# Performance work log

Hardware: AMD Instinct MI355X
Metric: run time of the kernel (lower is better)

Reference implementation:

```python
import jax, jax.numpy as jnp
import numpy as np

SIGMA_SPATIAL = 1.0
SIGMA_BILATERAL = 0.25
RADIUS = 1
PATCH = 2 * RADIUS + 1  # 3


def _spatial_kernel():
    x, y = np.mgrid[-RADIUS:RADIUS + 1, -RADIUS:RADIUS + 1]
    w1 = np.exp(-(x ** 2 + y ** 2) / (2.0 * SIGMA_SPATIAL ** 2))
    return jnp.asarray(w1.reshape(-1), dtype=jnp.float32)  # [PATCH*PATCH]


def _extract_patches(x):
    # x: [B,H,W,C] -> [B,H,W,PATCH*PATCH,C] via reflect-padded shifted slices
    B, H, W, C = x.shape
    xp = jnp.pad(x, ((0, 0), (RADIUS, RADIUS), (RADIUS, RADIUS), (0, 0)), mode='reflect')
    return jnp.stack(
        [xp[:, dy:dy + H, dx:dx + W, :] for dy in range(PATCH) for dx in range(PATCH)],
        axis=3,
    )


def setup_inputs() -> dict:
    key = jax.random.key(0)
    k1, k2 = jax.random.split(key)
    src = jax.random.uniform(k1, (2, 512, 512, 21), dtype=jnp.float32)
    im = jax.random.uniform(k2, (2, 512, 512, 3), dtype=jnp.float32)
    return {"src": src, "im": im}


def reference(src, im):
    w1 = _spatial_kernel()  # [9]
    im_patches = _extract_patches(im)                      # [B,H,W,9,Ci]
    diff2 = jnp.sum((im_patches - im[:, :, :, None, :]) ** 2, axis=-1)  # [B,H,W,9]
    w = jnp.exp(-diff2 / (2.0 * SIGMA_BILATERAL ** 2)) * w1            # [B,H,W,9]
    src_patches = _extract_patches(src)                    # [B,H,W,9,Cs]
    num = jnp.sum(src_patches * w[..., None], axis=3)      # [B,H,W,Cs]
    den = jnp.sum(w, axis=3, keepdims=True)                # [B,H,W,1]
    return num / den
```

## Files before the change

kernel.cpp:

```cpp
#include <hip/hip_runtime.h>

#define BATCH 2
#define H 512
#define W 512
#define CS 21
#define CI 3
#define P 64
#define TPB 256

__device__ __forceinline__ int reflect1(int v, int n) {
    if (v < 0) v = -v;
    else if (v >= n) v = 2 * n - 2 - v;
    return v;
}

__global__ __launch_bounds__(TPB) void jbu_kernel(
    const float* __restrict__ src, const float* __restrict__ im,
    float* __restrict__ out)
{
    __shared__ float s_im[3][P + 2][CI];
    __shared__ float s_w[P * 9];
    __shared__ float s_invden[P];

    const int t  = threadIdx.x;
    const int x0 = blockIdx.x * P;
    const int y  = blockIdx.y;
    const int b  = blockIdx.z;

    const int ry0 = reflect1(y - 1, H);
    const int ry2 = reflect1(y + 1, H);
    const int ryr[3] = { ry0, y, ry2 };

    for (int i = t; i < 3 * (P + 2) * CI; i += TPB) {
        int r   = i / ((P + 2) * CI);
        int rem = i - r * ((P + 2) * CI);
        int col = rem / CI;
        int ch  = rem - col * CI;
        int gx  = reflect1(x0 + col - 1, W);
        s_im[r][col][ch] = im[((b * H + ryr[r]) * W + gx) * CI + ch];
    }
    __syncthreads();

    const float w1[9] = {0.36787944f, 0.60653066f, 0.36787944f,
                         0.60653066f, 1.0f,        0.60653066f,
                         0.36787944f, 0.60653066f, 0.36787944f};

    for (int s = t; s < P * 9; s += TPB) {
        int p  = s / 9;
        int k  = s - p * 9;
        int dy = k / 3;
        int dx = k - dy * 3;
        float d0 = s_im[dy][p + dx][0] - s_im[1][p + 1][0];
        float d1 = s_im[dy][p + dx][1] - s_im[1][p + 1][1];
        float d2 = s_im[dy][p + dx][2] - s_im[1][p + 1][2];
        float dist2 = d0 * d0 + d1 * d1 + d2 * d2;
        s_w[s] = __expf(-8.0f * dist2) * w1[k];
    }
    __syncthreads();

    if (t < P) {
        float den = 0.f;
        #pragma unroll
        for (int k = 0; k < 9; ++k) den += s_w[t * 9 + k];
        s_invden[t] = 1.0f / den;
    }
    __syncthreads();

    const long rowb0 = (long)(b * H + ry0) * W;
    const long rowb1 = (long)(b * H + y  ) * W;
    const long rowb2 = (long)(b * H + ry2) * W;

    for (int e = t; e < P * CS; e += TPB) {
        int p = e / CS;
        int c = e - p * CS;
        int x = x0 + p;
        int xm = reflect1(x - 1, W);
        int xp = reflect1(x + 1, W);
        const float* wp = &s_w[p * 9];
        float acc;
        acc  = src[(rowb0 + xm) * CS + c] * wp[0];
        acc += src[(rowb0 + x ) * CS + c] * wp[1];
        acc += src[(rowb0 + xp) * CS + c] * wp[2];
        acc += src[(rowb1 + xm) * CS + c] * wp[3];
        acc += src[(rowb1 + x ) * CS + c] * wp[4];
        acc += src[(rowb1 + xp) * CS + c] * wp[5];
        acc += src[(rowb2 + xm) * CS + c] * wp[6];
        acc += src[(rowb2 + x ) * CS + c] * wp[7];
        acc += src[(rowb2 + xp) * CS + c] * wp[8];
        out[(rowb1 + x) * CS + c] = acc * s_invden[p];
    }
}

extern "C" void kernel_launch(void* const* d_in, const int* in_sizes, int n_in,
                              void* d_out, int out_size, void* d_ws, size_t ws_size,
                              hipStream_t stream) {
    const float* src = (const float*)d_in[0];
    const float* im  = (const float*)d_in[1];
    float* out = (float*)d_out;
    dim3 grid(W / P, H, BATCH);
    jbu_kernel<<<grid, TPB, 0, stream>>>(src, im, out);
}
```

Baseline: 126.1 us.

## Vectorize source stencil with float4 chunks and fold normalization into weights

Each block now covers 256 pixels instead of 64, so one thread owns one pixel. Each thread computes its 9 bilateral weights and their normalized values in registers, which removes a separate denominator pass and one barrier. The gather of the 21 source channels becomes 6 float4 chunks per pixel, with the last chunk starting at channel 17 and overlapping the previous one. The goal is to cut the number of global load and store instructions and the redundant scalar index arithmetic. Because 21 channels is odd, the float4 accesses are not 16-byte aligned, so this relies on the hardware handling unaligned vector loads and stores. Channels 17 to 19 are also written twice with identical values.

```diff
diff --git a/kernel.cpp b/kernel.cpp
--- a/kernel.cpp
+++ b/kernel.cpp
@@ -5,8 +5,9 @@
 #define W 512
 #define CS 21
 #define CI 3
-#define P 64
+#define P 256
 #define TPB 256
+#define NCH 6
 
 __device__ __forceinline__ int reflect1(int v, int n) {
     if (v < 0) v = -v;
@@ -14,13 +15,19 @@
     return v;
 }
 
+__device__ __forceinline__ void fma4(float4& a, const float4 v, const float w) {
+    a.x = fmaf(v.x, w, a.x);
+    a.y = fmaf(v.y, w, a.y);
+    a.z = fmaf(v.z, w, a.z);
+    a.w = fmaf(v.w, w, a.w);
+}
+
 __global__ __launch_bounds__(TPB) void jbu_kernel(
     const float* __restrict__ src, const float* __restrict__ im,
     float* __restrict__ out)
 {
-    __shared__ float s_im[3][P + 2][CI];
-    __shared__ float s_w[P * 9];
-    __shared__ float s_invden[P];
+    __shared__ __align__(16) float s_im[3][P + 2][CI];
+    __shared__ __align__(16) float s_w[P][12];
 
     const int t  = threadIdx.x;
     const int x0 = blockIdx.x * P;
@@ -29,65 +36,88 @@
 
     const int ry0 = reflect1(y - 1, H);
     const int ry2 = reflect1(y + 1, H);
-    const int ryr[3] = { ry0, y, ry2 };
 
     for (int i = t; i < 3 * (P + 2) * CI; i += TPB) {
         int r   = i / ((P + 2) * CI);
         int rem = i - r * ((P + 2) * CI);
         int col = rem / CI;
         int ch  = rem - col * CI;
+        int ry  = (r == 0) ? ry0 : ((r == 1) ? y : ry2);
         int gx  = reflect1(x0 + col - 1, W);
-        s_im[r][col][ch] = im[((b * H + ryr[r]) * W + gx) * CI + ch];
+        s_im[r][col][ch] = im[((b * H + ry) * W + gx) * CI + ch];
     }
     __syncthreads();
 
-    const float w1[9] = {0.36787944f, 0.60653066f, 0.36787944f,
-                         0.60653066f, 1.0f,        0.60653066f,
-                         0.36787944f, 0.60653066f, 0.36787944f};
-
-    for (int s = t; s < P * 9; s += TPB) {
-        int p  = s / 9;
-        int k  = s - p * 9;
-        int dy = k / 3;
-        int dx = k - dy * 3;
-        float d0 = s_im[dy][p + dx][0] - s_im[1][p + 1][0];
-        float d1 = s_im[dy][p + dx][1] - s_im[1][p + 1][1];
-        float d2 = s_im[dy][p + dx][2] - s_im[1][p + 1][2];
-        float dist2 = d0 * d0 + d1 * d1 + d2 * d2;
-        s_w[s] = __expf(-8.0f * dist2) * w1[k];
+    {
+        const float w1k[9] = {0.36787944f, 0.60653066f, 0.36787944f,
+                              0.60653066f, 1.0f,        0.60653066f,
+                              0.36787944f, 0.60653066f, 0.36787944f};
+        const float c0 = s_im[1][t + 1][0];
+        const float c1 = s_im[1][t + 1][1];
+        const float c2 = s_im[1][t + 1][2];
+        float wv[9];
+        float den = 0.f;
+        #pragma unroll
+        for (int k = 0; k < 9; ++k) {
+            const int dy = k / 3, dx = k % 3;
+            float d0 = s_im[dy][t + dx][0] - c0;
+            float d1 = s_im[dy][t + dx][1] - c1;
+            float d2 = s_im[dy][t + dx][2] - c2;
+            float w = __expf(-8.0f * (d0 * d0 + d1 * d1 + d2 * d2)) * w1k[k];
+            wv[k] = w;
+            den += w;
+        }
+        const float inv = 1.0f / den;
+        float4 wa = {wv[0] * inv, wv[1] * inv, wv[2] * inv, wv[3] * inv};
+        float4 wb = {wv[4] * inv, wv[5] * inv, wv[6] * inv, wv[7] * inv};
+        *(float4*)&s_w[t][0] = wa;
+        *(float4*)&s_w[t][4] = wb;
+        s_w[t][8] = wv[8] * inv;
     }
     __syncthreads();
 
-    if (t < P) {
-        float den = 0.f;
-        #pragma unroll
-        for (int k = 0; k < 9; ++k) den += s_w[t * 9 + k];
-        s_invden[t] = 1.0f / den;
-    }
-    __syncthreads();
+    const float* row0 = src + (size_t)(b * H + ry0) * (W * CS);
+    const float* row1 = src + (size_t)(b * H + y  ) * (W * CS);
+    const float* row2 = src + (size_t)(b * H + ry2) * (W * CS);
+    float*       orow = out + (size_t)(b * H + y  ) * (W * CS);
 
-    const long rowb0 = (long)(b * H + ry0) * W;
-    const long rowb1 = (long)(b * H + y  ) * W;
-    const long rowb2 = (long)(b * H + ry2) * W;
+    for (int wi = t; wi < P * NCH; wi += TPB) {
+        int p = wi / NCH;
+        int q = wi - p * NCH;
+        int coff = (q == 5) ? 17 : (q << 2);
+        int x  = x0 + p;
+        int xm = (x == 0)     ? 1     : x - 1;
+        int xp = (x == W - 1) ? W - 2 : x + 1;
+        int om = xm * CS + coff;
+        int oc = x  * CS + coff;
+        int op = xp * CS + coff;
 
-    for (int e = t; e < P * CS; e += TPB) {
-        int p = e / CS;
-        int c = e - p * CS;
-        int x = x0 + p;
-        int xm = reflect1(x - 1, W);
-        int xp = reflect1(x + 1, W);
-        const float* wp = &s_w[p * 9];
-        float acc;
-        acc  = src[(rowb0 + xm) * CS + c] * wp[0];
-        acc += src[(rowb0 + x ) * CS + c] * wp[1];
-        acc += src[(rowb0 + xp) * CS + c] * wp[2];
-        acc += src[(rowb1 + xm) * CS + c] * wp[3];
-        acc += src[(rowb1 + x ) * CS + c] * wp[4];
-        acc += src[(rowb1 + xp) * CS + c] * wp[5];
-        acc += src[(rowb2 + xm) * CS + c] * wp[6];
-        acc += src[(rowb2 + x ) * CS + c] * wp[7];
-        acc += src[(rowb2 + xp) * CS + c] * wp[8];
-        out[(rowb1 + x) * CS + c] = acc * s_invden[p];
+        const float4 wA = *(const float4*)&s_w[p][0];
+        const float4 wB = *(const float4*)&s_w[p][4];
+        const float  w8 = s_w[p][8];
+
+        float4 v0 = *(const float4*)(row0 + om);
+        float4 v1 = *(const float4*)(row0 + oc);
+        float4 v2 = *(const float4*)(row0 + op);
+        float4 v3 = *(const float4*)(row1 + om);
+        float4 v4 = *(const float4*)(row1 + oc);
+        float4 v5 = *(const float4*)(row1 + op);
+        float4 v6 = *(const float4*)(row2 + om);
+        float4 v7 = *(const float4*)(row2 + oc);
+        float4 v8 = *(const float4*)(row2 + op);
+
+        float4 acc = {0.f, 0.f, 0.f, 0.f};
+        fma4(acc, v0, wA.x);
+        fma4(acc, v1, wA.y);
+        fma4(acc, v2, wA.z);
+        fma4(acc, v3, wA.w);
+        fma4(acc, v4, wB.x);
+        fma4(acc, v5, wB.y);
+        fma4(acc, v6, wB.z);
+        fma4(acc, v7, wB.w);
+        fma4(acc, v8, w8);
+
+        *(float4*)(orow + oc) = acc;
     }
 }
 
```

Result: faster. 114.7 us (-9.0%).
